# Kernel optimization log

Hardware: AMD Instinct MI355X
Metric: run time of the kernel (lower is better)

The kernel has to match this reference:

```python
import jax, jax.numpy as jnp
import numpy as np

E = 2048   # embed_dim
H = 16     # num query heads
D = E // H # head_dim = 128
B = 2
S = 2048


def setup_inputs() -> dict:
    key = jax.random.key(0)
    ks = jax.random.split(key, 12)
    sc = 0.02
    return {
        "input": jax.random.normal(ks[0], (B, S, E), jnp.float32),
        "kv": jax.random.normal(ks[1], (B, S, E), jnp.float32),
        "Wq": jax.random.normal(ks[2], (E, E), jnp.float32) * sc,
        "bq": jnp.zeros((E,), jnp.float32),
        "Wk": jax.random.normal(ks[3], (D, E), jnp.float32) * sc,
        "bk": jnp.zeros((D,), jnp.float32),
        "Wv": jax.random.normal(ks[4], (D, E), jnp.float32) * sc,
        "bv": jnp.zeros((D,), jnp.float32),
        "Wo": jax.random.normal(ks[5], (E, E), jnp.float32) * sc,
        "bo": jnp.zeros((E,), jnp.float32),
        "expanding_context": 0,
    }


def reference(input, kv, Wq, bq, Wk, bk, Wv, bv, Wo, bo, expanding_context):
    b, s, _ = input.shape
    # projections (torch Linear: x @ W.T + b)
    q = (input @ Wq.T + bq).reshape(b, s, H, D).transpose(0, 2, 1, 3)  # [B,H,S,D]
    k = kv @ Wk.T + bk  # [B,S,D] single KV head
    v = kv @ Wv.T + bv  # [B,S,D]
    # scores with single KV head broadcast across query heads
    scores = jnp.einsum('bhsd,btd->bhst', q, k) / jnp.sqrt(jnp.float32(D))
    causal = jnp.triu(jnp.ones((s, s), bool), k=1)  # True above diagonal
    scores = jnp.where(causal[None, None], jnp.float32(-jnp.inf), scores)
    attn = jax.nn.softmax(scores, axis=-1)
    out = jnp.einsum('bhst,btd->bhsd', attn, v)  # [B,H,S,D]
    out = out.transpose(0, 2, 1, 3).reshape(b, s, E)
    return out @ Wo.T + bo
```

## Files before the change

kernel.cpp:

```cpp
#include <hip/hip_runtime.h>

#define B_  2
#define S_  2048
#define E_  2048
#define H_  16
#define D_  128
#define BS_ (B_*S_)

typedef __bf16 bf16_t;
typedef __bf16 bf16x8 __attribute__((ext_vector_type(8)));
typedef __bf16 bf16x4 __attribute__((ext_vector_type(4)));
typedef float  f32x4  __attribute__((ext_vector_type(4)));

#define QSCALE 0.1275174131003543f

__device__ __forceinline__ void gld16(const bf16_t* g, bf16_t* l) {
    __builtin_amdgcn_global_load_lds(
        (const __attribute__((address_space(1))) void*)g,
        (__attribute__((address_space(3))) void*)l,
        16, 0, 0);
}

__global__ void cvt_all(const float* __restrict__ s0, const float* __restrict__ s1,
                        const float* __restrict__ s2, const float* __restrict__ s3,
                        const float* __restrict__ s4, const float* __restrict__ s5,
                        bf16_t* d0, bf16_t* d1, bf16_t* d2,
                        bf16_t* d3, bf16_t* d4, bf16_t* d5)
{
    long i = ((long)blockIdx.x * blockDim.x + threadIdx.x) * 4;
    const float* s; bf16_t* d;
    if      (i <  8388608) { s = s0; d = d0; }
    else if (i < 16777216) { s = s1; d = d1; i -=  8388608; }
    else if (i < 20971520) { s = s2; d = d2; i -= 16777216; }
    else if (i < 21233664) { s = s3; d = d3; i -= 20971520; }
    else if (i < 21495808) { s = s4; d = d4; i -= 21233664; }
    else                   { s = s5; d = d5; i -= 21495808; }
    float4 v = *(const float4*)(s + i);
    bf16x4 o;
    o[0] = (bf16_t)v.x; o[1] = (bf16_t)v.y; o[2] = (bf16_t)v.z; o[3] = (bf16_t)v.w;
    *(bf16x4*)(d + i) = o;
}

template<int EP>
__device__ __forceinline__ void gemm_tile64(
    const bf16_t* __restrict__ A, const bf16_t* __restrict__ W,
    const float* __restrict__ biasA, const float* __restrict__ biasB,
    float* __restrict__ Cf, bf16_t* __restrict__ Cb,
    int N, int K, float scale, int m0, int w_n0, int c_n0,
    bf16_t* As, bf16_t* Bs)
{
    const int tid  = threadIdx.x;
    const int wave = tid >> 6, lane = tid & 63;
    const int wm = wave >> 1, wn = wave & 1;
    const int lrow = lane & 15, quad = lane >> 4;
    const int r8 = lane >> 3, c8 = (lane & 7) << 3;

    f32x4 acc[4][2] = {};

    for (int k0 = 0; k0 < K; k0 += 64) {
        __syncthreads();
#pragma unroll
        for (int j = 0; j < 4; ++j) {
            int base = (wave * 4 + j) * 8;
            gld16(A + (size_t)(m0 + base + r8) * K + k0 + c8, &As[base * 64]);
        }
#pragma unroll
        for (int j = 0; j < 2; ++j) {
            int base = (wave * 2 + j) * 8;
            gld16(W + (size_t)(w_n0 + base + r8) * K + k0 + c8, &Bs[base * 64]);
        }
        __syncthreads();
#pragma unroll
        for (int ks = 0; ks < 2; ++ks) {
            bf16x8 af[4], bfr[2];
#pragma unroll
            for (int mt = 0; mt < 4; ++mt)
                af[mt] = *(const bf16x8*)&As[(wm * 64 + mt * 16 + lrow) * 64 + ks * 32 + quad * 8];
#pragma unroll
            for (int nt = 0; nt < 2; ++nt)
                bfr[nt] = *(const bf16x8*)&Bs[(wn * 32 + nt * 16 + lrow) * 64 + ks * 32 + quad * 8];
#pragma unroll
            for (int mt = 0; mt < 4; ++mt)
#pragma unroll
                for (int nt = 0; nt < 2; ++nt)
                    acc[mt][nt] = __builtin_amdgcn_mfma_f32_16x16x32_bf16(
                        af[mt], bfr[nt], acc[mt][nt], 0, 0, 0);
        }
    }

#pragma unroll
    for (int mt = 0; mt < 4; ++mt) {
#pragma unroll
        for (int nt = 0; nt < 2; ++nt) {
            int nn = wn * 32 + nt * 16 + lrow;
            int col = c_n0 + nn;
            float bvv = (EP == 1 && biasB && col >= 128) ? biasB[col - 128]
                                                         : biasA[col];
#pragma unroll
            for (int r = 0; r < 4; ++r) {
                int row = m0 + wm * 64 + mt * 16 + quad * 4 + r;
                float v = (acc[mt][nt][r] + bvv) * scale;
                if (EP == 0) Cf[(size_t)row * N + col] = v;
                else         Cb[(size_t)row * N + col] = (bf16_t)v;
            }
        }
    }
}

__global__ __launch_bounds__(256) void gemm_qkv(
    const bf16_t* __restrict__ xb, const bf16_t* __restrict__ kvb,
    const bf16_t* __restrict__ Wq, const bf16_t* __restrict__ Wkv,
    const float* __restrict__ bq, const float* __restrict__ bk,
    const float* __restrict__ bv,
    bf16_t* __restrict__ Qb, bf16_t* __restrict__ KVb)
{
    __shared__ __align__(16) bf16_t As[128 * 64];
    __shared__ __align__(16) bf16_t Bs[64 * 64];
    const int m0 = blockIdx.y * 128;
    if (blockIdx.x < 32) {
        int n0 = blockIdx.x * 64;
        gemm_tile64<1>(xb, Wq, bq, nullptr, nullptr, Qb, E_, E_, QSCALE,
                       m0, n0, n0, As, Bs);
    } else {
        int n0 = (blockIdx.x - 32) * 64;
        gemm_tile64<1>(kvb, Wkv, bk, bv, nullptr, KVb, 256, E_, 1.0f,
                       m0, n0, n0, As, Bs);
    }
}

__global__ __launch_bounds__(256) void gemm_o(
    const bf16_t* __restrict__ A, const bf16_t* __restrict__ W,
    const float* __restrict__ bias, float* __restrict__ Cf)
{
    __shared__ __align__(16) bf16_t As[128 * 64];
    __shared__ __align__(16) bf16_t Bs[64 * 64];
    int n0 = blockIdx.x * 64;
    gemm_tile64<0>(A, W, bias, nullptr, Cf, nullptr, E_, E_, 1.0f,
                   blockIdx.y * 128, n0, n0, As, Bs);
}

__global__ __launch_bounds__(512, 4) void mqa_attn(
    const bf16_t* __restrict__ Q, const bf16_t* __restrict__ KV,
    bf16_t* __restrict__ O)
{
    __shared__ __align__(16) bf16_t Kt[64][136];
    __shared__ __align__(16) bf16_t Vt[128][72];
    __shared__ __align__(16) bf16_t Pl[8][16][72];

    const int bx = blockIdx.x, h = blockIdx.y, b = blockIdx.z;
    const int qb = b ? bx : (15 - bx);
    const int tid = threadIdx.x, wave = tid >> 6, lane = tid & 63;
    const int lrow = lane & 15, quad = lane >> 4;
    const int q0 = qb * 128 + wave * 16;

    const bf16_t* kvp = KV + (size_t)(b * S_) * 256;

    bf16x8 qf[4];
    {
        const bf16_t* qp = Q + ((size_t)(b * S_ + q0 + lrow)) * E_ + h * D_ + quad * 8;
#pragma unroll
        for (int ks = 0; ks < 4; ++ks) qf[ks] = *(const bf16x8*)(qp + ks * 32);
    }

    f32x4 oacc[8] = {};
    float rs[4] = {0.f, 0.f, 0.f, 0.f};

    const int ntiles = 2 * qb + 2;
    bf16x8 kreg[2], vreg[2];

#pragma unroll
    for (int i = 0; i < 2; ++i) {
        int c = tid + 512 * i;
        kreg[i] = *(const bf16x8*)(kvp + (size_t)(c >> 4) * 256 + ((c & 15) << 3));
        vreg[i] = *(const bf16x8*)(kvp + (size_t)(c & 63) * 256 + 128 + ((c >> 6) << 3));
    }

    for (int kt = 0; kt < ntiles; ++kt) {
        const int k_base = kt * 64;
        __syncthreads();
#pragma unroll
        for (int i = 0; i < 2; ++i) {
            int c = tid + 512 * i;
            *(bf16x8*)&Kt[c >> 4][(c & 15) << 3] = kreg[i];
            int n = c & 63, d0 = (c >> 6) << 3;
#pragma unroll
            for (int j = 0; j < 8; ++j) Vt[d0 + j][n] = vreg[i][j];
        }
        __syncthreads();
        if (kt + 1 < ntiles) {
            const int nb = (kt + 1) * 64;
#pragma unroll
            for (int i = 0; i < 2; ++i) {
                int c = tid + 512 * i;
                kreg[i] = *(const bf16x8*)(kvp + (size_t)(nb + (c >> 4)) * 256 + ((c & 15) << 3));
                vreg[i] = *(const bf16x8*)(kvp + (size_t)(nb + (c & 63)) * 256 + 128 + ((c >> 6) << 3));
            }
        }

        if (k_base <= q0 + 15) {
            f32x4 sc[4] = {};
#pragma unroll
            for (int ks = 0; ks < 4; ++ks) {
                bf16x8 a = qf[ks];
#pragma unroll
                for (int c = 0; c < 4; ++c) {
                    bf16x8 kb = *(const bf16x8*)&Kt[c * 16 + lrow][ks * 32 + quad * 8];
                    sc[c] = __builtin_amdgcn_mfma_f32_16x16x32_bf16(a, kb, sc[c], 0, 0, 0);
                }
            }
            const bool diag = (k_base + 63 > q0);
#pragma unroll
            for (int c = 0; c < 4; ++c) {
#pragma unroll
                for (int r = 0; r < 4; ++r) {
                    float s = sc[c][r];
                    if (diag) {
                        int kj = k_base + c * 16 + lrow;
                        int qi = q0 + quad * 4 + r;
                        if (kj > qi) s = -1e30f;
                    }
                    float p = exp2f(fminf(s, 110.f));
                    rs[r] += p;
                    Pl[wave][quad * 4 + r][c * 16 + lrow] = (bf16_t)p;
                }
            }
#pragma unroll
            for (int ks = 0; ks < 2; ++ks) {
                bf16x8 ap = *(const bf16x8*)&Pl[wave][lrow][ks * 32 + quad * 8];
#pragma unroll
                for (int dt = 0; dt < 8; ++dt) {
                    bf16x8 bv = *(const bf16x8*)&Vt[dt * 16 + lrow][ks * 32 + quad * 8];
                    oacc[dt] = __builtin_amdgcn_mfma_f32_16x16x32_bf16(ap, bv, oacc[dt], 0, 0, 0);
                }
            }
        }
    }

#pragma unroll
    for (int off = 8; off >= 1; off >>= 1)
#pragma unroll
        for (int r = 0; r < 4; ++r) rs[r] += __shfl_xor(rs[r], off, 16);
#pragma unroll
    for (int r = 0; r < 4; ++r) {
        float inv = 1.0f / rs[r];
        int row = q0 + quad * 4 + r;
#pragma unroll
        for (int dt = 0; dt < 8; ++dt)
            O[((size_t)(b * S_ + row)) * E_ + h * D_ + dt * 16 + lrow] =
                (bf16_t)(oacc[dt][r] * inv);
    }
}

extern "C" void kernel_launch(void* const* d_in, const int* in_sizes, int n_in,
                              void* d_out, int out_size, void* d_ws, size_t ws_size,
                              hipStream_t stream)
{
    const float* x   = (const float*)d_in[0];
    const float* kv  = (const float*)d_in[1];
    const float* Wq  = (const float*)d_in[2];
    const float* bq  = (const float*)d_in[3];
    const float* Wk  = (const float*)d_in[4];
    const float* bk  = (const float*)d_in[5];
    const float* Wv  = (const float*)d_in[6];
    const float* bv  = (const float*)d_in[7];
    const float* Wo  = (const float*)d_in[8];
    const float* bo  = (const float*)d_in[9];
    float* out = (float*)d_out;

    bf16_t* p    = (bf16_t*)d_ws;
    bf16_t* xb   = p;  p += (size_t)BS_ * E_;
    bf16_t* kvb  = p;  p += (size_t)BS_ * E_;
    bf16_t* Wqb  = p;  p += (size_t)E_ * E_;
    bf16_t* Wkvb = p;  p += (size_t)2 * D_ * E_;
    bf16_t* Wob  = p;  p += (size_t)E_ * E_;
    bf16_t* Qb   = p;  p += (size_t)BS_ * E_;
    bf16_t* KVb  = p;  p += (size_t)BS_ * 256;
    bf16_t* Ob   = p;  p += (size_t)BS_ * E_;

    cvt_all<<<dim3(25088), dim3(256), 0, stream>>>(
        x, kv, Wq, Wk, Wv, Wo,
        xb, kvb, Wqb, Wkvb, Wkvb + (size_t)D_ * E_, Wob);

    gemm_qkv<<<dim3(36, BS_ / 128), 256, 0, stream>>>(
        xb, kvb, Wqb, Wkvb, bq, bk, bv, Qb, KVb);

    mqa_attn<<<dim3(S_ / 128, H_, B_), 512, 0, stream>>>(Qb, KVb, Ob);

    gemm_o<<<dim3(E_ / 64, BS_ / 128), 256, 0, stream>>>(Ob, Wob, bo, out);
}
```

Before: 366.5 us.

## Switch MQA attention to 32x32 MFMA with register-resident P via lane shuffles

Rewrites the attention kernel to use 256-thread blocks where each wave handles 32 query rows with 32x32x16 bf16 MFMAs, computing S^T so the probabilities stay in registers. The P matrix is repacked to the A-operand layout with cross-half-wave shuffles instead of going through shared memory, which removes the Pl LDS round trip. Row sums go through a small LDS buffer for the final normalisation. The aim is fewer LDS accesses and more work per MFMA. The cost is higher register pressure (f32x16 accumulators) and half as many waves per block.

```diff
diff --git a/kernel.cpp b/kernel.cpp
--- a/kernel.cpp
+++ b/kernel.cpp
@@ -11,6 +11,7 @@
 typedef __bf16 bf16x8 __attribute__((ext_vector_type(8)));
 typedef __bf16 bf16x4 __attribute__((ext_vector_type(4)));
 typedef float  f32x4  __attribute__((ext_vector_type(4)));
+typedef float  f32x16 __attribute__((ext_vector_type(16)));
 
 #define QSCALE 0.1275174131003543f
 
@@ -139,38 +140,38 @@
                    blockIdx.y * 128, n0, n0, As, Bs);
 }
 
-__global__ __launch_bounds__(512, 4) void mqa_attn(
+__global__ __launch_bounds__(256, 2) void mqa_attn(
     const bf16_t* __restrict__ Q, const bf16_t* __restrict__ KV,
     bf16_t* __restrict__ O)
 {
     __shared__ __align__(16) bf16_t Kt[64][136];
     __shared__ __align__(16) bf16_t Vt[128][72];
-    __shared__ __align__(16) bf16_t Pl[8][16][72];
+    __shared__ float rsl[4][32];
 
     const int bx = blockIdx.x, h = blockIdx.y, b = blockIdx.z;
     const int qb = b ? bx : (15 - bx);
     const int tid = threadIdx.x, wave = tid >> 6, lane = tid & 63;
-    const int lrow = lane & 15, quad = lane >> 4;
-    const int q0 = qb * 128 + wave * 16;
+    const int ln = lane & 31, hi = lane >> 5;
+    const int q0w = qb * 128 + wave * 32;
 
     const bf16_t* kvp = KV + (size_t)(b * S_) * 256;
 
-    bf16x8 qf[4];
+    bf16x8 qf[8];
     {
-        const bf16_t* qp = Q + ((size_t)(b * S_ + q0 + lrow)) * E_ + h * D_ + quad * 8;
-#pragma unroll
-        for (int ks = 0; ks < 4; ++ks) qf[ks] = *(const bf16x8*)(qp + ks * 32);
-    }
-
-    f32x4 oacc[8] = {};
-    float rs[4] = {0.f, 0.f, 0.f, 0.f};
+        const bf16_t* qp = Q + ((size_t)(b * S_ + q0w + ln)) * E_ + h * D_ + hi * 8;
+#pragma unroll
+        for (int st = 0; st < 8; ++st) qf[st] = *(const bf16x8*)(qp + st * 16);
+    }
+
+    f32x16 oacc[4] = {};
+    float rs = 0.f;
 
     const int ntiles = 2 * qb + 2;
-    bf16x8 kreg[2], vreg[2];
-
-#pragma unroll
-    for (int i = 0; i < 2; ++i) {
-        int c = tid + 512 * i;
+    bf16x8 kreg[4], vreg[4];
+
+#pragma unroll
+    for (int i = 0; i < 4; ++i) {
+        int c = tid + 256 * i;
         kreg[i] = *(const bf16x8*)(kvp + (size_t)(c >> 4) * 256 + ((c & 15) << 3));
         vreg[i] = *(const bf16x8*)(kvp + (size_t)(c & 63) * 256 + 128 + ((c >> 6) << 3));
     }
@@ -179,8 +180,8 @@
         const int k_base = kt * 64;
         __syncthreads();
 #pragma unroll
-        for (int i = 0; i < 2; ++i) {
-            int c = tid + 512 * i;
+        for (int i = 0; i < 4; ++i) {
+            int c = tid + 256 * i;
             *(bf16x8*)&Kt[c >> 4][(c & 15) << 3] = kreg[i];
             int n = c & 63, d0 = (c >> 6) << 3;
 #pragma unroll
@@ -190,65 +191,83 @@
         if (kt + 1 < ntiles) {
             const int nb = (kt + 1) * 64;
 #pragma unroll
-            for (int i = 0; i < 2; ++i) {
-                int c = tid + 512 * i;
+            for (int i = 0; i < 4; ++i) {
+                int c = tid + 256 * i;
                 kreg[i] = *(const bf16x8*)(kvp + (size_t)(nb + (c >> 4)) * 256 + ((c & 15) << 3));
                 vreg[i] = *(const bf16x8*)(kvp + (size_t)(nb + (c & 63)) * 256 + 128 + ((c >> 6) << 3));
             }
         }
 
-        if (k_base <= q0 + 15) {
-            f32x4 sc[4] = {};
-#pragma unroll
-            for (int ks = 0; ks < 4; ++ks) {
-                bf16x8 a = qf[ks];
-#pragma unroll
-                for (int c = 0; c < 4; ++c) {
-                    bf16x8 kb = *(const bf16x8*)&Kt[c * 16 + lrow][ks * 32 + quad * 8];
-                    sc[c] = __builtin_amdgcn_mfma_f32_16x16x32_bf16(a, kb, sc[c], 0, 0, 0);
+        if (k_base <= q0w + 31) {
+            f32x16 sc[2] = {f32x16{}, f32x16{}};
+#pragma unroll
+            for (int st = 0; st < 8; ++st) {
+                bf16x8 qv = qf[st];
+#pragma unroll
+                for (int ct = 0; ct < 2; ++ct) {
+                    bf16x8 kf = *(const bf16x8*)&Kt[ct * 32 + ln][st * 16 + hi * 8];
+                    sc[ct] = __builtin_amdgcn_mfma_f32_32x32x16_bf16(kf, qv, sc[ct], 0, 0, 0);
                 }
             }
-            const bool diag = (k_base + 63 > q0);
-#pragma unroll
-            for (int c = 0; c < 4; ++c) {
-#pragma unroll
-                for (int r = 0; r < 4; ++r) {
-                    float s = sc[c][r];
+            const int qi = q0w + ln;
+            const bool diag = (k_base + 63 > q0w);
+#pragma unroll
+            for (int ct = 0; ct < 2; ++ct) {
+#pragma unroll
+                for (int r = 0; r < 16; ++r) {
+                    float s = sc[ct][r];
                     if (diag) {
-                        int kj = k_base + c * 16 + lrow;
-                        int qi = q0 + quad * 4 + r;
+                        int kj = k_base + ct * 32 + (r & 3) + 8 * (r >> 2) + 4 * hi;
                         if (kj > qi) s = -1e30f;
                     }
                     float p = exp2f(fminf(s, 110.f));
-                    rs[r] += p;
-                    Pl[wave][quad * 4 + r][c * 16 + lrow] = (bf16_t)p;
+                    rs += p;
+                    sc[ct][r] = p;
                 }
             }
-#pragma unroll
-            for (int ks = 0; ks < 2; ++ks) {
-                bf16x8 ap = *(const bf16x8*)&Pl[wave][lrow][ks * 32 + quad * 8];
-#pragma unroll
-                for (int dt = 0; dt < 8; ++dt) {
-                    bf16x8 bv = *(const bf16x8*)&Vt[dt * 16 + lrow][ks * 32 + quad * 8];
-                    oacc[dt] = __builtin_amdgcn_mfma_f32_16x16x32_bf16(ap, bv, oacc[dt], 0, 0, 0);
+            bf16x8 af[4];
+#pragma unroll
+            for (int ks = 0; ks < 4; ++ks) {
+                const int c = ks >> 1, b8 = (ks & 1) * 8;
+                union { bf16_t h[2]; unsigned u; } pk0, pk1, pk2, pk3;
+                pk0.h[0] = (bf16_t)sc[c][b8 + 0]; pk0.h[1] = (bf16_t)sc[c][b8 + 1];
+                pk1.h[0] = (bf16_t)sc[c][b8 + 2]; pk1.h[1] = (bf16_t)sc[c][b8 + 3];
+                pk2.h[0] = (bf16_t)sc[c][b8 + 4]; pk2.h[1] = (bf16_t)sc[c][b8 + 5];
+                pk3.h[0] = (bf16_t)sc[c][b8 + 6]; pk3.h[1] = (bf16_t)sc[c][b8 + 7];
+                const unsigned U0 = pk0.u, U1 = pk1.u, U2 = pk2.u, U3 = pk3.u;
+                const unsigned V0 = __shfl_xor(U0, 32);
+                const unsigned V1 = __shfl_xor(U1, 32);
+                const unsigned V2 = __shfl_xor(U2, 32);
+                const unsigned V3 = __shfl_xor(U3, 32);
+                union { unsigned u[4]; bf16x8 v; } W;
+                W.u[0] = hi ? V2 : U0;
+                W.u[1] = hi ? V3 : U1;
+                W.u[2] = hi ? U2 : V0;
+                W.u[3] = hi ? U3 : V1;
+                af[ks] = W.v;
+            }
+#pragma unroll
+            for (int ks = 0; ks < 4; ++ks)
+#pragma unroll
+                for (int t = 0; t < 4; ++t) {
+                    bf16x8 vf = *(const bf16x8*)&Vt[t * 32 + ln][ks * 16 + hi * 8];
+                    oacc[t] = __builtin_amdgcn_mfma_f32_32x32x16_bf16(af[ks], vf, oacc[t], 0, 0, 0);
                 }
-            }
-        }
-    }
-
-#pragma unroll
-    for (int off = 8; off >= 1; off >>= 1)
-#pragma unroll
-        for (int r = 0; r < 4; ++r) rs[r] += __shfl_xor(rs[r], off, 16);
-#pragma unroll
-    for (int r = 0; r < 4; ++r) {
-        float inv = 1.0f / rs[r];
-        int row = q0 + quad * 4 + r;
-#pragma unroll
-        for (int dt = 0; dt < 8; ++dt)
-            O[((size_t)(b * S_ + row)) * E_ + h * D_ + dt * 16 + lrow] =
-                (bf16_t)(oacc[dt][r] * inv);
-    }
+        }
+    }
+
+    rs += __shfl_xor(rs, 32);
+    __syncthreads();
+    if (lane < 32) rsl[wave][ln] = 1.0f / rs;
+    __syncthreads();
+#pragma unroll
+    for (int t = 0; t < 4; ++t)
+#pragma unroll
+        for (int r = 0; r < 16; ++r) {
+            int ro = (r & 3) + 8 * (r >> 2) + 4 * hi;
+            O[((size_t)(b * S_ + q0w + ro)) * E_ + h * D_ + t * 32 + ln] =
+                (bf16_t)(oacc[t][r] * rsl[wave][ro]);
+        }
 }
 
 extern "C" void kernel_launch(void* const* d_in, const int* in_sizes, int n_in,
@@ -284,7 +303,7 @@
     gemm_qkv<<<dim3(36, BS_ / 128), 256, 0, stream>>>(
         xb, kvb, Wqb, Wkvb, bq, bk, bv, Qb, KVb);
 
-    mqa_attn<<<dim3(S_ / 128, H_, B_), 512, 0, stream>>>(Qb, KVb, Ob);
+    mqa_attn<<<dim3(S_ / 128, H_, B_), 256, 0, stream>>>(Qb, KVb, Ob);
 
     gemm_o<<<dim3(E_ / 64, BS_ / 128), 256, 0, stream>>>(Ob, Wob, bo, out);
 }
```

New measurement: 358.5 us. 1.02x faster.
